# Performance work log

Measured on AMD Instinct MI355X. Metric: run time of the kernel, lower is better.

## Reference

```python
import jax, jax.numpy as jnp
import numpy as np

T, P, N = 16, 250000, 20  # steps, n_params, n_inputs


def setup_inputs() -> dict:
    key = jax.random.key(0)
    ks = jax.random.split(key, 7)
    x_all = jax.random.normal(ks[0], (T, P, N), dtype=jnp.float32)          # [steps, n_params, n_inputs]
    grad = jax.random.normal(ks[1], (T,), dtype=jnp.float32) * 0.1           # one learner-grad scalar per step (grad[i])
    WF = jax.random.normal(ks[2], (N + 2, 1), dtype=jnp.float32) * 0.05      # forget-gate weights
    WI = jax.random.normal(ks[3], (N + 2, 1), dtype=jnp.float32) * 0.05      # input-gate weights
    cI = jax.random.normal(ks[4], (P, 1), dtype=jnp.float32) * 0.05          # initial cell state (flat learner params)
    bF = jax.random.uniform(ks[5], (1, 1), minval=8.0, maxval=10.0, dtype=jnp.float32)
    bI = jax.random.uniform(ks[6], (1, 1), minval=-5.0, maxval=-4.0, dtype=jnp.float32)
    return {"x_all": x_all, "grad": grad, "WF": WF, "WI": WI, "cI": cI, "bF": bF, "bI": bI}


def reference(x_all, grad, WF, WI, cI, bF, bI):
    n_params = x_all.shape[1]
    f0 = jnp.zeros((n_params, 1), dtype=x_all.dtype)
    i0 = jnp.zeros((n_params, 1), dtype=x_all.dtype)

    def step(carry, inp):
        f_prev, i_prev, c_prev = carry
        x_t, g_t = inp  # x_t: [P, N], g_t: scalar
        f_next = jnp.concatenate([x_t, c_prev, f_prev], axis=1) @ WF + bF  # [P, 1]
        i_next = jnp.concatenate([x_t, c_prev, i_prev], axis=1) @ WI + bI  # [P, 1]
        c_next = jax.nn.sigmoid(f_next) * c_prev - jax.nn.sigmoid(i_next) * g_t
        return (f_next, i_next, c_next), None

    (f_T, i_T, c_T), _ = jax.lax.scan(step, (f0, i0, cI), (x_all, grad))
    # original returns (cx, [f, i, cx])
    return (c_T, f_T, i_T)
```

## Files before the change

### kernel.cpp

```cpp
#include <hip/hip_runtime.h>


#define BLOCK 256
#define N_IN 20
#define ROW_F4 5

__global__ __launch_bounds__(BLOCK) void metalstm_kernel(
    const float* __restrict__ x_all,
    const float* __restrict__ grad,
    const float* __restrict__ WF,
    const float* __restrict__ WI,
    const float* __restrict__ cI,
    const float* __restrict__ bF,
    const float* __restrict__ bI,
    float* __restrict__ out,
    int P, int T)
{
    __shared__ __align__(16) float4 xs4[BLOCK * ROW_F4];

    const int tid = threadIdx.x;
    const int pbase = blockIdx.x * BLOCK;
    const int p = pbase + tid;
    const bool valid = (p < P);
    const int pc = valid ? p : (P - 1);

    float wF[22], wI[22];
#pragma unroll
    for (int k = 0; k < 22; ++k) { wF[k] = WF[k]; wI[k] = WI[k]; }
    const float biasF = bF[0];
    const float biasI = bI[0];

    float f = 0.0f;
    float ii = 0.0f;
    float c = cI[pc];

    const float4* __restrict__ x4 = reinterpret_cast<const float4*>(x_all);

    float4 pr0, pr1, pr2, pr3, pr4;
    {
        const long base4 = (long)P * 0 * ROW_F4 + (long)pbase * ROW_F4;
        const long end4  = ((long)P * 0 + P) * ROW_F4;
#define LOADK(k, dst) { long idx = base4 + tid + (k) * BLOCK; \
                        if (idx >= end4) idx = end4 - 1; \
                        dst = x4[idx]; }
        LOADK(0, pr0) LOADK(1, pr1) LOADK(2, pr2) LOADK(3, pr3) LOADK(4, pr4)
    }

    for (int t = 0; t < T; ++t) {
        __syncthreads();

#define STOREK(k, src) { const int fidx = tid + (k) * BLOCK; \
                         const int row = fidx / ROW_F4; \
                         const int sl  = fidx - row * ROW_F4; \
                         int slr = sl + row % ROW_F4; if (slr >= ROW_F4) slr -= ROW_F4; \
                         xs4[row * ROW_F4 + slr] = src; }
        STOREK(0, pr0) STOREK(1, pr1) STOREK(2, pr2) STOREK(3, pr3) STOREK(4, pr4)
#undef STOREK
        __syncthreads();

        if (t + 1 < T) {
            const long base4 = ((long)(t + 1) * P + pbase) * ROW_F4;
            const long end4  = ((long)(t + 1) * P + P) * ROW_F4;
            LOADK(0, pr0) LOADK(1, pr1) LOADK(2, pr2) LOADK(3, pr3) LOADK(4, pr4)
        }

        const float g_t = grad[t];

        float dF = biasF, dI = biasI;
        const int rbase = tid * ROW_F4;
        const int rrot  = tid % ROW_F4;
#define ACC4(jj) { int slr = (jj) + rrot; if (slr >= ROW_F4) slr -= ROW_F4; \
                   const float4 v = xs4[rbase + slr]; \
                   dF = fmaf(v.x, wF[4*(jj)+0], dF); dI = fmaf(v.x, wI[4*(jj)+0], dI); \
                   dF = fmaf(v.y, wF[4*(jj)+1], dF); dI = fmaf(v.y, wI[4*(jj)+1], dI); \
                   dF = fmaf(v.z, wF[4*(jj)+2], dF); dI = fmaf(v.z, wI[4*(jj)+2], dI); \
                   dF = fmaf(v.w, wF[4*(jj)+3], dF); dI = fmaf(v.w, wI[4*(jj)+3], dI); }
        ACC4(0) ACC4(1) ACC4(2) ACC4(3) ACC4(4)
#undef ACC4

        const float fn  = fmaf(c, wF[20], fmaf(f,  wF[21], dF));
        const float in_ = fmaf(c, wI[20], fmaf(ii, wI[21], dI));
        const float sf = 1.0f / (1.0f + __expf(-fn));
        const float si = 1.0f / (1.0f + __expf(-in_));
        c = sf * c - si * g_t;
        f = fn;
        ii = in_;
    }
#undef LOADK

    if (valid) {
        out[p]         = c;
        out[P + p]     = f;
        out[2 * P + p] = ii;
    }
}

extern "C" void kernel_launch(void* const* d_in, const int* in_sizes, int n_in,
                              void* d_out, int out_size, void* d_ws, size_t ws_size,
                              hipStream_t stream) {
    const float* x_all = (const float*)d_in[0];
    const float* grad  = (const float*)d_in[1];
    const float* WF    = (const float*)d_in[2];
    const float* WI    = (const float*)d_in[3];
    const float* cI    = (const float*)d_in[4];
    const float* bF    = (const float*)d_in[5];
    const float* bI    = (const float*)d_in[6];
    float* out = (float*)d_out;

    const int P = in_sizes[4];
    const int T = in_sizes[1];
    const int grid = (P + BLOCK - 1) / BLOCK;
    metalstm_kernel<<<grid, BLOCK, 0, stream>>>(x_all, grad, WF, WI, cI, bF, bI, out, P, T);
}
```

Baseline: 55.77 us.

## Stream x tiles directly into double-buffered LDS via global_load_lds

Input rows now go from global memory straight into LDS with the async global_load_lds builtin, which writes 16 bytes per lane. Per-lane source addresses are pre-permuted so the LDS layout keeps the existing rotation swizzle. Two LDS buffers let the next step's tile load while the current one is computed, and each step now needs one barrier instead of two. This drops the register staging and the separate LDS store pass. It relies on the barrier waiting for the async LDS writes to finish, and it doubles the LDS footprint per block.

```diff
diff --git a/kernel.cpp b/kernel.cpp
--- a/kernel.cpp
+++ b/kernel.cpp
@@ -4,6 +4,10 @@
 #define BLOCK 256
 #define N_IN 20
 #define ROW_F4 5
+#define SLAB_F4 (BLOCK * ROW_F4)
+
+#define AS_GLOBAL(p) ((const __attribute__((address_space(1))) void*)(const void*)(p))
+#define AS_LDS(p)    ((__attribute__((address_space(3))) void*)(void*)(p))
 
 __global__ __launch_bounds__(BLOCK) void metalstm_kernel(
     const float* __restrict__ x_all,
@@ -16,9 +20,11 @@
     float* __restrict__ out,
     int P, int T)
 {
-    __shared__ __align__(16) float4 xs4[BLOCK * ROW_F4];
+    __shared__ __align__(16) float4 xs4[2][SLAB_F4];
 
     const int tid = threadIdx.x;
+    const int w = tid >> 6;
+    const int l = tid & 63;
     const int pbase = blockIdx.x * BLOCK;
     const int p = pbase + tid;
     const bool valid = (p < P);
@@ -30,47 +36,46 @@
     const float biasF = bF[0];
     const float biasI = bI[0];
 
+    const char* __restrict__ xbytes = (const char*)x_all;
+    const long stepBytes = (long)P * (N_IN * 4);
+#define MKSRC(k, ptrvar) const char* ptrvar; { \
+        const int q = (k) * BLOCK + w * 64 + l; \
+        const int row = q / ROW_F4; \
+        int slot = (q - row * ROW_F4) - (row % ROW_F4); \
+        if (slot < 0) slot += ROW_F4; \
+        int srcrow = pbase + row; if (srcrow >= P) srcrow = P - 1; \
+        ptrvar = xbytes + ((long)srcrow * ROW_F4 + slot) * 16; }
+    MKSRC(0, src0) MKSRC(1, src1) MKSRC(2, src2) MKSRC(3, src3) MKSRC(4, src4)
+#undef MKSRC
+
+#define ISSUE(bufidx) { \
+        __builtin_amdgcn_global_load_lds(AS_GLOBAL(src0), AS_LDS(&xs4[bufidx][0 * BLOCK + w * 64]), 16, 0, 0); \
+        __builtin_amdgcn_global_load_lds(AS_GLOBAL(src1), AS_LDS(&xs4[bufidx][1 * BLOCK + w * 64]), 16, 0, 0); \
+        __builtin_amdgcn_global_load_lds(AS_GLOBAL(src2), AS_LDS(&xs4[bufidx][2 * BLOCK + w * 64]), 16, 0, 0); \
+        __builtin_amdgcn_global_load_lds(AS_GLOBAL(src3), AS_LDS(&xs4[bufidx][3 * BLOCK + w * 64]), 16, 0, 0); \
+        __builtin_amdgcn_global_load_lds(AS_GLOBAL(src4), AS_LDS(&xs4[bufidx][4 * BLOCK + w * 64]), 16, 0, 0); \
+        src0 += stepBytes; src1 += stepBytes; src2 += stepBytes; \
+        src3 += stepBytes; src4 += stepBytes; }
+
     float f = 0.0f;
     float ii = 0.0f;
     float c = cI[pc];
 
-    const float4* __restrict__ x4 = reinterpret_cast<const float4*>(x_all);
+    ISSUE(0)
+    __syncthreads();
 
-    float4 pr0, pr1, pr2, pr3, pr4;
-    {
-        const long base4 = (long)P * 0 * ROW_F4 + (long)pbase * ROW_F4;
-        const long end4  = ((long)P * 0 + P) * ROW_F4;
-#define LOADK(k, dst) { long idx = base4 + tid + (k) * BLOCK; \
-                        if (idx >= end4) idx = end4 - 1; \
-                        dst = x4[idx]; }
-        LOADK(0, pr0) LOADK(1, pr1) LOADK(2, pr2) LOADK(3, pr3) LOADK(4, pr4)
-    }
+    const int rbase = tid * ROW_F4;
+    const int rrot = tid % ROW_F4;
 
     for (int t = 0; t < T; ++t) {
-        __syncthreads();
-
-#define STOREK(k, src) { const int fidx = tid + (k) * BLOCK; \
-                         const int row = fidx / ROW_F4; \
-                         const int sl  = fidx - row * ROW_F4; \
-                         int slr = sl + row % ROW_F4; if (slr >= ROW_F4) slr -= ROW_F4; \
-                         xs4[row * ROW_F4 + slr] = src; }
-        STOREK(0, pr0) STOREK(1, pr1) STOREK(2, pr2) STOREK(3, pr3) STOREK(4, pr4)
-#undef STOREK
-        __syncthreads();
-
-        if (t + 1 < T) {
-            const long base4 = ((long)(t + 1) * P + pbase) * ROW_F4;
-            const long end4  = ((long)(t + 1) * P + P) * ROW_F4;
-            LOADK(0, pr0) LOADK(1, pr1) LOADK(2, pr2) LOADK(3, pr3) LOADK(4, pr4)
-        }
+        const int cur = t & 1;
+        if (t + 1 < T) { ISSUE(cur ^ 1) }
 
         const float g_t = grad[t];
 
         float dF = biasF, dI = biasI;
-        const int rbase = tid * ROW_F4;
-        const int rrot  = tid % ROW_F4;
 #define ACC4(jj) { int slr = (jj) + rrot; if (slr >= ROW_F4) slr -= ROW_F4; \
-                   const float4 v = xs4[rbase + slr]; \
+                   const float4 v = xs4[cur][rbase + slr]; \
                    dF = fmaf(v.x, wF[4*(jj)+0], dF); dI = fmaf(v.x, wI[4*(jj)+0], dI); \
                    dF = fmaf(v.y, wF[4*(jj)+1], dF); dI = fmaf(v.y, wI[4*(jj)+1], dI); \
                    dF = fmaf(v.z, wF[4*(jj)+2], dF); dI = fmaf(v.z, wI[4*(jj)+2], dI); \
@@ -85,8 +90,10 @@
         c = sf * c - si * g_t;
         f = fn;
         ii = in_;
+
+        __syncthreads();
     }
-#undef LOADK
+#undef ISSUE
 
     if (valid) {
         out[p]         = c;
```

Measured after the change: 57.87 us. 1.04x slower.

## Use per-wave LDS slabs to drop block-wide barriers in staging

Applied to the files above, without the earlier changes.

Each wavefront now stages its own 64 rows of x into a private LDS slab and synchronizes with only an lgkmcnt wait instead of two block-wide __syncthreads per step. The bank-conflict rotation is removed, index math moves to 32-bit unsigned offsets, and sched_barriers pin the ordering of stores, the next prefetch and the reads. This removes cross-wave barrier stalls, but the unrotated stride-5 float4 LDS reads may conflict, and 32-bit indexing limits the maximum input size.

```diff
diff --git a/kernel.cpp b/kernel.cpp
--- a/kernel.cpp
+++ b/kernel.cpp
@@ -2,8 +2,10 @@
 
 
 #define BLOCK 256
+#define NWAVE (BLOCK / 64)
 #define N_IN 20
 #define ROW_F4 5
+#define WSLAB (64 * ROW_F4)
 
 __global__ __launch_bounds__(BLOCK) void metalstm_kernel(
     const float* __restrict__ x_all,
@@ -16,11 +18,12 @@
     float* __restrict__ out,
     int P, int T)
 {
-    __shared__ __align__(16) float4 xs4[BLOCK * ROW_F4];
+    __shared__ __align__(16) float4 xs4[NWAVE][WSLAB];
 
     const int tid = threadIdx.x;
-    const int pbase = blockIdx.x * BLOCK;
-    const int p = pbase + tid;
+    const int w = tid >> 6;
+    const int l = tid & 63;
+    const int p = blockIdx.x * BLOCK + tid;
     const bool valid = (p < P);
     const int pc = valid ? p : (P - 1);
 
@@ -30,53 +33,54 @@
     const float biasF = bF[0];
     const float biasI = bI[0];
 
+    const int wrow0 = blockIdx.x * BLOCK + (w << 6);
+    const float4* __restrict__ x4 = reinterpret_cast<const float4*>(x_all);
+
+    const unsigned stepF4 = (unsigned)P * ROW_F4;
+    unsigned base4 = (unsigned)wrow0 * ROW_F4;
+    unsigned end4  = stepF4;
+
+    float4 pr0, pr1, pr2, pr3, pr4;
+#define PREF() { \
+    unsigned i0 = base4 + 0 * 64 + l; if (i0 >= end4) i0 = end4 - 1; \
+    unsigned i1 = base4 + 1 * 64 + l; if (i1 >= end4) i1 = end4 - 1; \
+    unsigned i2 = base4 + 2 * 64 + l; if (i2 >= end4) i2 = end4 - 1; \
+    unsigned i3 = base4 + 3 * 64 + l; if (i3 >= end4) i3 = end4 - 1; \
+    unsigned i4 = base4 + 4 * 64 + l; if (i4 >= end4) i4 = end4 - 1; \
+    pr0 = x4[i0]; pr1 = x4[i1]; pr2 = x4[i2]; pr3 = x4[i3]; pr4 = x4[i4]; }
+
+    PREF()
+
     float f = 0.0f;
     float ii = 0.0f;
     float c = cI[pc];
 
-    const float4* __restrict__ x4 = reinterpret_cast<const float4*>(x_all);
+    for (int t = 0; t < T; ++t) {
+        __builtin_amdgcn_sched_barrier(0);
 
-    float4 pr0, pr1, pr2, pr3, pr4;
-    {
-        const long base4 = (long)P * 0 * ROW_F4 + (long)pbase * ROW_F4;
-        const long end4  = ((long)P * 0 + P) * ROW_F4;
-#define LOADK(k, dst) { long idx = base4 + tid + (k) * BLOCK; \
-                        if (idx >= end4) idx = end4 - 1; \
-                        dst = x4[idx]; }
-        LOADK(0, pr0) LOADK(1, pr1) LOADK(2, pr2) LOADK(3, pr3) LOADK(4, pr4)
-    }
+        xs4[w][0 * 64 + l] = pr0;
+        xs4[w][1 * 64 + l] = pr1;
+        xs4[w][2 * 64 + l] = pr2;
+        xs4[w][3 * 64 + l] = pr3;
+        xs4[w][4 * 64 + l] = pr4;
+        asm volatile("s_waitcnt lgkmcnt(0)" ::: "memory");
+        __builtin_amdgcn_sched_barrier(0);
 
-    for (int t = 0; t < T; ++t) {
-        __syncthreads();
-
-#define STOREK(k, src) { const int fidx = tid + (k) * BLOCK; \
-                         const int row = fidx / ROW_F4; \
-                         const int sl  = fidx - row * ROW_F4; \
-                         int slr = sl + row % ROW_F4; if (slr >= ROW_F4) slr -= ROW_F4; \
-                         xs4[row * ROW_F4 + slr] = src; }
-        STOREK(0, pr0) STOREK(1, pr1) STOREK(2, pr2) STOREK(3, pr3) STOREK(4, pr4)
-#undef STOREK
-        __syncthreads();
-
-        if (t + 1 < T) {
-            const long base4 = ((long)(t + 1) * P + pbase) * ROW_F4;
-            const long end4  = ((long)(t + 1) * P + P) * ROW_F4;
-            LOADK(0, pr0) LOADK(1, pr1) LOADK(2, pr2) LOADK(3, pr3) LOADK(4, pr4)
-        }
+        if (t + 1 < T) { base4 += stepF4; end4 += stepF4; PREF() }
 
         const float g_t = grad[t];
 
         float dF = biasF, dI = biasI;
-        const int rbase = tid * ROW_F4;
-        const int rrot  = tid % ROW_F4;
-#define ACC4(jj) { int slr = (jj) + rrot; if (slr >= ROW_F4) slr -= ROW_F4; \
-                   const float4 v = xs4[rbase + slr]; \
-                   dF = fmaf(v.x, wF[4*(jj)+0], dF); dI = fmaf(v.x, wI[4*(jj)+0], dI); \
-                   dF = fmaf(v.y, wF[4*(jj)+1], dF); dI = fmaf(v.y, wI[4*(jj)+1], dI); \
-                   dF = fmaf(v.z, wF[4*(jj)+2], dF); dI = fmaf(v.z, wI[4*(jj)+2], dI); \
-                   dF = fmaf(v.w, wF[4*(jj)+3], dF); dI = fmaf(v.w, wI[4*(jj)+3], dI); }
-        ACC4(0) ACC4(1) ACC4(2) ACC4(3) ACC4(4)
-#undef ACC4
+        const int rb = l * ROW_F4;
+#pragma unroll
+        for (int jj = 0; jj < ROW_F4; ++jj) {
+            const float4 v = xs4[w][rb + jj];
+            dF = fmaf(v.x, wF[4 * jj + 0], dF); dI = fmaf(v.x, wI[4 * jj + 0], dI);
+            dF = fmaf(v.y, wF[4 * jj + 1], dF); dI = fmaf(v.y, wI[4 * jj + 1], dI);
+            dF = fmaf(v.z, wF[4 * jj + 2], dF); dI = fmaf(v.z, wI[4 * jj + 2], dI);
+            dF = fmaf(v.w, wF[4 * jj + 3], dF); dI = fmaf(v.w, wI[4 * jj + 3], dI);
+        }
+#undef PREF
 
         const float fn  = fmaf(c, wF[20], fmaf(f,  wF[21], dF));
         const float in_ = fmaf(c, wI[20], fmaf(ii, wI[21], dI));
@@ -86,7 +90,6 @@
         f = fn;
         ii = in_;
     }
-#undef LOADK
 
     if (valid) {
         out[p]         = c;
```

New measurement: 56.02 us. Within noise of the previous version (+0.4%).
